# Optimization experiments

Measured on AMD Instinct MI355X. Metric: run time of the kernel, lower is better.

Reference implementation:

```python
import jax, jax.numpy as jnp
import numpy as np
import math

N_FFT = 1024
HOP = 256
WIN = 1024
SR = 16000
N_MELS = 80
N_STFT = N_FFT // 2 + 1  # 513
B = 16
T_AUDIO = 320000


def _hz_to_mel_slaney(f):
    f = np.asarray(f, dtype=np.float64)
    mels = 3.0 * f / 200.0
    min_log_hz = 1000.0
    min_log_mel = 15.0
    logstep = math.log(6.4) / 27.0
    return np.where(f >= min_log_hz, min_log_mel + np.log(np.maximum(f, 1e-10) / min_log_hz) / logstep, mels)


def _mel_to_hz_slaney(m):
    m = np.asarray(m, dtype=np.float64)
    freqs = 200.0 * m / 3.0
    min_log_hz = 1000.0
    min_log_mel = 15.0
    logstep = math.log(6.4) / 27.0
    return np.where(m >= min_log_mel, min_log_hz * np.exp(logstep * (m - min_log_mel)), freqs)


def _melscale_fbanks(n_freqs, f_min, f_max, n_mels, sample_rate):
    # torchaudio.functional.melscale_fbanks with norm='slaney', mel_scale='slaney'
    all_freqs = np.linspace(0.0, sample_rate / 2.0, n_freqs)
    m_pts = np.linspace(_hz_to_mel_slaney(f_min), _hz_to_mel_slaney(f_max), n_mels + 2)
    f_pts = _mel_to_hz_slaney(m_pts)
    f_diff = f_pts[1:] - f_pts[:-1]                       # (n_mels+1,)
    slopes = f_pts[None, :] - all_freqs[:, None]          # (n_freqs, n_mels+2)
    down = -slopes[:, :-2] / f_diff[:-1]
    up = slopes[:, 2:] / f_diff[1:]
    fb = np.maximum(0.0, np.minimum(down, up))
    enorm = 2.0 / (f_pts[2:n_mels + 2] - f_pts[:n_mels])  # slaney norm
    fb = fb * enorm[None, :]
    return fb.astype(np.float32)                          # (n_freqs, n_mels)


def setup_inputs() -> dict:
    key = jax.random.key(0)
    wav = jax.random.normal(key, (B, 1, T_AUDIO), dtype=jnp.float32)
    # hann window, periodic
    n = np.arange(WIN, dtype=np.float64)
    window = (0.5 - 0.5 * np.cos(2.0 * np.pi * n / WIN)).astype(np.float32)
    mel_fbanks = _melscale_fbanks(N_STFT, 0.0, SR / 2.0, N_MELS, SR)
    k = np.arange(N_STFT, dtype=np.float64)[:, None]
    nn = np.arange(N_FFT, dtype=np.float64)[None, :]
    angle = -2.0 * np.pi * k * nn / N_FFT
    rfft_real_t = np.cos(angle).T.astype(np.float32)      # (n_fft, n_stft)
    rfft_imag_t = np.sin(angle).T.astype(np.float32)
    return {
        "wav_with_channel": wav,
        "window": jnp.asarray(window),
        "mel_fbanks": jnp.asarray(mel_fbanks),
        "rfft_real_t": jnp.asarray(rfft_real_t),
        "rfft_imag_t": jnp.asarray(rfft_imag_t),
    }


def reference(wav_with_channel, window, mel_fbanks, rfft_real_t, rfft_imag_t):
    wav = wav_with_channel[:, 0, :]                       # (B, T)
    pad = N_FFT // 2
    padded = jnp.pad(wav, ((0, 0), (pad, pad)), mode="reflect")
    padded_len = padded.shape[1]
    num_frames = (padded_len - WIN) // HOP + 1
    idx = jnp.arange(num_frames)[:, None] * HOP + jnp.arange(WIN)[None, :]
    frames = padded[:, idx]
    windowed = frames * window
    real = jnp.matmul(windowed, rfft_real_t)              # (B, F, n_stft)
    imag = jnp.matmul(windowed, rfft_imag_t)
    magnitude = jnp.sqrt(real * real + imag * imag)       # power == 1.0
    mel = jnp.matmul(magnitude, mel_fbanks)               # (B, F, n_mels)
    return jnp.transpose(mel, (0, 2, 1))                  # (B, n_mels, F)
```

## Files before the change

kernel.cpp:

```cpp
#include <hip/hip_runtime.h>
#include <cstddef>

#define HOP 256
#define NSTFT 513
#define N_MELS 80
#define T_AUDIO 320000
#define NUM_FRAMES 1251
#define NBATCH 16
#define TOTAL_FRAMES (NBATCH * NUM_FRAMES)

#define LOGSTEP 0.06875177742094913f
#define MEL_MAX 45.24564047f
#define DF 15.625f

__device__ __forceinline__ int reflect_idx(int j) {
    j = (j < 0) ? -j : j;
    j = (j >= T_AUDIO) ? (2 * T_AUDIO - 2 - j) : j;
    return j;
}

__device__ __forceinline__ int m1_of(int k) {
    const float f = k * DF;
    const float mel = (f < 1000.f) ? (3.0f / 200.0f) * f
                                   : 15.0f + logf(f * 1e-3f) * (1.0f / LOGSTEP);
    return (int)floorf(mel * (81.0f / MEL_MAX));
}

__device__ __forceinline__ int swz(int k) {
    return (k & ~15) | ((k ^ (k >> 4)) & 15);
}

__device__ __forceinline__ unsigned cvt_pk_bf16(float lo, float hi) {
    unsigned r;
    asm("v_cvt_pk_bf16_f32 %0, %1, %2" : "=v"(r) : "v"(lo), "v"(hi));
    return r;
}

__device__ __forceinline__ float plsum32(float v) {
#if __has_builtin(__builtin_amdgcn_permlane32_swap)
    auto r = __builtin_amdgcn_permlane32_swap(__float_as_int(v), __float_as_int(v), false, false);
    return __int_as_float(r[0]) + __int_as_float(r[1]);
#else
    return v + __shfl_xor(v, 32);
#endif
}
__device__ __forceinline__ float plsum16(float v) {
#if __has_builtin(__builtin_amdgcn_permlane16_swap)
    auto r = __builtin_amdgcn_permlane16_swap(__float_as_int(v), __float_as_int(v), false, false);
    return __int_as_float(r[0]) + __int_as_float(r[1]);
#else
    return v + __shfl_xor(v, 16);
#endif
}

#define DPP_XOR1 0xB1
#define DPP_XOR2 0x4E
#define DPP_XOR8 0x128
template<int CTRL>
__device__ __forceinline__ float dppf(float x) {
    return __int_as_float(__builtin_amdgcn_update_dpp(
        0, __float_as_int(x), CTRL, 0xF, 0xF, true));
}

template<class F>
__device__ __forceinline__ void cstage(float (&zr)[2][16], float (&zi)[2][16],
                                       float sg, float twr_, float twi_, F comm) {
    #pragma unroll
    for (int p = 0; p < 2; ++p) {
        #pragma unroll
        for (int r = 0; r < 16; ++r) {
            const float pr  = comm(zr[p][r]);
            const float pim = comm(zi[p][r]);
            const float qr = fmaf(sg, zr[p][r], pr);
            const float qi = fmaf(sg, zi[p][r], pim);
            zr[p][r] = fmaf(qr, twr_, -(qi * twi_));
            zi[p][r] = fmaf(qr, twi_, qi * twr_);
        }
    }
}

template<class FS>
__device__ __forceinline__ void cstage_sum(float (&zr)[2][16], float (&zi)[2][16],
                                           float m2, float twr_, float twi_, FS sumf) {
    #pragma unroll
    for (int p = 0; p < 2; ++p) {
        #pragma unroll
        for (int r = 0; r < 16; ++r) {
            const float sR = sumf(zr[p][r]);
            const float sI = sumf(zi[p][r]);
            const float qr = fmaf(m2, zr[p][r], sR);
            const float qi = fmaf(m2, zi[p][r], sI);
            zr[p][r] = fmaf(qr, twr_, -(qi * twi_));
            zi[p][r] = fmaf(qr, twi_, qi * twr_);
        }
    }
}

__global__ __launch_bounds__(256) void melspec_pk4_kernel(
    const float* __restrict__ wav,
    const float* __restrict__ window,
    const float* __restrict__ fb,
    const float* __restrict__ cosT,
    const float* __restrict__ sinT,
    float* __restrict__ out)
{
    __shared__ uint2  smag4[4][512];
    __shared__ float2 wtab[512];
    __shared__ unsigned short ks[84];

    const int tid = threadIdx.x;
    const int lane = tid & 63;
    const int w = tid >> 6;
    const int g0 = (blockIdx.x * 4 + w) * 4;

    const int BREV4[16] = {0,8,4,12,2,10,6,14,1,9,5,13,3,11,7,15};
    const int SIG[16]   = {0,1,3,2,7,6,5,4,15,14,13,12,11,10,9,8};
    const float W16R[8] = {1.0f, 0.92387953251128674f, 0.70710678118654752f, 0.38268343236508977f,
                           0.0f, -0.38268343236508977f, -0.70710678118654752f, -0.92387953251128674f};
    const float W16I[8] = {0.0f, -0.38268343236508977f, -0.70710678118654752f, -0.92387953251128674f,
                           -1.0f, -0.92387953251128674f, -0.70710678118654752f, -0.38268343236508977f};

    if (tid == 0) { ks[81] = 512; ks[82] = 512; }
    for (int k = tid; k <= 512; k += 256) {
        const int mc = m1_of(k);
        if (k <= 511) {
            const float wu = (mc >= 0 && mc <= 79) ? fb[k * N_MELS + mc] : 0.0f;
            const float wd = (mc >= 1 && mc <= 80) ? fb[k * N_MELS + mc - 1] : 0.0f;
            wtab[swz(k)] = make_float2(wu, wd);
        }
        if (k >= 1) {
            const int mp = m1_of(k - 1);
            for (int m = mp + 1; m <= mc; ++m) ks[m] = (unsigned short)k;
            if (k == 1) ks[0] = 1;
        }
    }
    __syncthreads();

    unsigned bf0, ff0, bf3;
    {
        const unsigned g = (unsigned)g0;
        bf0 = g / NUM_FRAMES; ff0 = g - bf0 * NUM_FRAMES;
        bf3 = (unsigned)(g0 + 3) / NUM_FRAMES;
    }

    float win[16];
    #pragma unroll
    for (int r = 0; r < 16; ++r) win[r] = window[r * 64 + lane];

    float zr[2][16], zi[2][16];
    if (bf0 == bf3) {
        const float* wb = wav + (size_t)bf0 * T_AUDIO;
        const int base = (int)ff0 * HOP - 512;
        float ch[28];
        if (base >= 0 && base + 27 * 64 + 63 < T_AUDIO) {
            #pragma unroll
            for (int c = 0; c < 28; ++c)
                ch[c] = wb[base + c * 64 + lane];
        } else {
            #pragma unroll
            for (int c = 0; c < 28; ++c)
                ch[c] = wb[reflect_idx(base + c * 64 + lane)];
        }
        #pragma unroll
        for (int r = 0; r < 16; ++r) {
            zr[0][r] = ch[r]      * win[r];
            zi[0][r] = ch[r + 4]  * win[r];
            zr[1][r] = ch[r + 8]  * win[r];
            zi[1][r] = ch[r + 12] * win[r];
        }
    } else {
        #pragma unroll
        for (int fi = 0; fi < 4; ++fi) {
            const unsigned g = (unsigned)(g0 + fi);
            const unsigned bb = g / NUM_FRAMES;
            const unsigned ffr = g - bb * NUM_FRAMES;
            const float* wb = wav + (size_t)bb * T_AUDIO;
            const int base = (int)ffr * HOP - 512;
            #pragma unroll
            for (int r = 0; r < 16; ++r) {
                const float v = wb[reflect_idx(base + r * 64 + lane)] * win[r];
                if (fi == 0) zr[0][r] = v;
                else if (fi == 1) zi[0][r] = v;
                else if (fi == 2) zr[1][r] = v;
                else zi[1][r] = v;
            }
        }
    }

    const float* twc = cosT + NSTFT;
    const float* tws = sinT + NSTFT;

    const float w1r = twc[lane];
    const float w1i = tws[lane];
    float wkr[16], wki[16];
    wkr[0] = 1.0f; wki[0] = 0.0f;
    #pragma unroll
    for (int k = 1; k < 16; ++k) {
        wkr[k] = wkr[k-1] * w1r - wki[k-1] * w1i;
        wki[k] = wkr[k-1] * w1i + wki[k-1] * w1r;
    }

    float c64[6], s64[6];
    #pragma unroll
    for (int t = 0; t < 6; ++t) {
        const int half = 32 >> t;
        const bool hi = (lane & half) != 0;
        const int jj = (lane & (half - 1)) << (t + 4);
        c64[t] = hi ? twc[jj] : 1.0f;
        s64[t] = hi ? tws[jj] : 0.0f;
    }

    #define CBFLY(ar, ai, br, bi, wr, wi) { \
        const float _tr = (ar) - (br), _ti = (ai) - (bi); \
        (ar) += (br); (ai) += (bi); \
        (br) = _tr * (wr) - _ti * (wi); \
        (bi) = _tr * (wi) + _ti * (wr); }

    #pragma unroll
    for (int p = 0; p < 2; ++p) {
        #pragma unroll
        for (int q = 0; q < 8; ++q) CBFLY(zr[p][q], zi[p][q], zr[p][q+8], zi[p][q+8], W16R[q], W16I[q]);
        #pragma unroll
        for (int g = 0; g < 16; g += 8)
            #pragma unroll
            for (int q = 0; q < 4; ++q) CBFLY(zr[p][g+q], zi[p][g+q], zr[p][g+q+4], zi[p][g+q+4], W16R[2*q], W16I[2*q]);
        #pragma unroll
        for (int g = 0; g < 16; g += 4)
            #pragma unroll
            for (int q = 0; q < 2; ++q) CBFLY(zr[p][g+q], zi[p][g+q], zr[p][g+q+2], zi[p][g+q+2], W16R[4*q], W16I[4*q]);
        #pragma unroll
        for (int g = 0; g < 16; g += 2) CBFLY(zr[p][g], zi[p][g], zr[p][g+1], zi[p][g+1], 1.0f, 0.0f);
    }

    #pragma unroll
    for (int r = 1; r < 16; ++r) {
        const float c1 = wkr[BREV4[r]];
        const float s1 = wki[BREV4[r]];
        #pragma unroll
        for (int p = 0; p < 2; ++p) {
            const float xr = zr[p][r], xi = zi[p][r];
            zr[p][r] = xr * c1 - xi * s1;
            zi[p][r] = xr * s1 + xi * c1;
        }
    }

    {
        cstage_sum(zr, zi, (lane & 32) ? -2.0f : 0.0f, c64[0], s64[0],
                   [](float v) { return plsum32(v); });
        cstage_sum(zr, zi, (lane & 16) ? -2.0f : 0.0f, c64[1], s64[1],
                   [](float v) { return plsum16(v); });
        float sg;
        sg = (lane & 8) ? -1.0f : 1.0f;
        cstage(zr, zi, sg, c64[2], s64[2], [](float v) { return dppf<DPP_XOR8>(v); });
        sg = (lane & 4) ? -1.0f : 1.0f;
        cstage(zr, zi, sg, c64[3], s64[3], [](float v) { return __shfl_xor(v, 4); });
        sg = (lane & 2) ? -1.0f : 1.0f;
        cstage(zr, zi, sg, c64[4], s64[4], [](float v) { return dppf<DPP_XOR2>(v); });
        sg = (lane & 1) ? -1.0f : 1.0f;
        cstage(zr, zi, sg, c64[5], s64[5], [](float v) { return dppf<DPP_XOR1>(v); });
    }

    const int k2 = (int)(__brev((unsigned)lane) >> 26);
    const int lp0 = (int)(__brev((unsigned)((64 - k2) & 63)) >> 26);
    #pragma unroll
    for (int r = 0; r < 16; ++r) {
        float cx0, cy0, cx1, cy1;
        if (r == 0) {
            cx0 = __shfl(zr[0][0], lp0); cy0 = __shfl(zi[0][0], lp0);
            cx1 = __shfl(zr[1][0], lp0); cy1 = __shfl(zi[1][0], lp0);
        } else {
            cx0 = __shfl_xor(zr[0][SIG[r]], 63); cy0 = __shfl_xor(zi[0][SIG[r]], 63);
            cx1 = __shfl_xor(zr[1][SIG[r]], 63); cy1 = __shfl_xor(zi[1][SIG[r]], 63);
        }
        const int k1 = BREV4[r];
        const int k = k2 * 16 + k1;
        if (k <= 511) {
            const float a0 = zr[0][r], b0 = zi[0][r];
            const float mA0 = 0.5f * sqrtf((a0 + cx0) * (a0 + cx0) + (b0 - cy0) * (b0 - cy0));
            const float mB0 = 0.5f * sqrtf((b0 + cy0) * (b0 + cy0) + (a0 - cx0) * (a0 - cx0));
            const float a1 = zr[1][r], b1 = zi[1][r];
            const float mA1 = 0.5f * sqrtf((a1 + cx1) * (a1 + cx1) + (b1 - cy1) * (b1 - cy1));
            const float mB1 = 0.5f * sqrtf((b1 + cy1) * (b1 + cy1) + (a1 - cx1) * (a1 - cx1));
            smag4[w][(k & ~15) | (k1 ^ (k2 & 15))] =
                make_uint2(cvt_pk_bf16(mA0, mB0), cvt_pk_bf16(mA1, mB1));
        }
    }

    #pragma unroll
    for (int ii = 0; ii < 3; ++ii) {
        const int t2 = lane + 64 * ii;
        if (t2 < 2 * N_MELS) {
            const int m = 79 - (t2 >> 1);
            const int half = t2 & 1;
            const int ka = ks[m], kb = ks[m + 1], kc = ks[m + 2];
            const int km = (ka + kc + 1) >> 1;
            const int kbeg = half ? km : ka;
            const int kend = half ? kc : km;
            float a0 = 0.f, b0 = 0.f, a1 = 0.f, b1 = 0.f;
            for (int k = kbeg; k < kend; ++k) {
                const int sl = swz(k);
                const uint2 mg = smag4[w][sl];
                const float2 wt = wtab[sl];
                const float ws = (k < kb) ? wt.x : wt.y;
                a0 = fmaf(__uint_as_float(mg.x << 16), ws, a0);
                b0 = fmaf(__uint_as_float(mg.x & 0xffff0000u), ws, b0);
                a1 = fmaf(__uint_as_float(mg.y << 16), ws, a1);
                b1 = fmaf(__uint_as_float(mg.y & 0xffff0000u), ws, b1);
            }
            a0 += dppf<DPP_XOR1>(a0);  b0 += dppf<DPP_XOR1>(b0);
            a1 += dppf<DPP_XOR1>(a1);  b1 += dppf<DPP_XOR1>(b1);
            const float v0 = half ? b0 : a0;
            const float v1 = half ? b1 : a1;
            const unsigned gA = (unsigned)(g0 + half);
            const unsigned bbA = gA / NUM_FRAMES;
            const unsigned ffA = gA - bbA * NUM_FRAMES;
            out[((size_t)bbA * N_MELS + m) * NUM_FRAMES + ffA] = v0;
            const unsigned gB = (unsigned)(g0 + 2 + half);
            const unsigned bbB = gB / NUM_FRAMES;
            const unsigned ffB = gB - bbB * NUM_FRAMES;
            out[((size_t)bbB * N_MELS + m) * NUM_FRAMES + ffB] = v1;
        }
    }
}

extern "C" void kernel_launch(void* const* d_in, const int* in_sizes, int n_in,
                              void* d_out, int out_size, void* d_ws, size_t ws_size,
                              hipStream_t stream) {
    const float* wav    = (const float*)d_in[0];
    const float* window = (const float*)d_in[1];
    const float* fb     = (const float*)d_in[2];
    const float* cosT   = (const float*)d_in[3];
    const float* sinT   = (const float*)d_in[4];
    float* out = (float*)d_out;

    const int blocks = TOTAL_FRAMES / 16;
    melspec_pk4_kernel<<<blocks, 256, 0, stream>>>(wav, window, fb, cosT, sinT, out);
}
```

Before: 46.64 us.

## Precompute mel weight tables in a setup kernel and use smaller blocks

After: 49.86 us. 6.9% more time.

```diff
diff --git a/kernel.cpp b/kernel.cpp
--- a/kernel.cpp
+++ b/kernel.cpp
@@ -35,6 +35,8 @@
     asm("v_cvt_pk_bf16_f32 %0, %1, %2" : "=v"(r) : "v"(lo), "v"(hi));
     return r;
 }
+__device__ __forceinline__ float lo16f(unsigned u) { return __uint_as_float(u << 16); }
+__device__ __forceinline__ float hi16f(unsigned u) { return __uint_as_float(u & 0xffff0000u); }
 
 __device__ __forceinline__ float plsum32(float v) {
 #if __has_builtin(__builtin_amdgcn_permlane32_swap)
@@ -96,13 +98,272 @@
     }
 }
 
-__global__ __launch_bounds__(256) void melspec_pk4_kernel(
+__global__ __launch_bounds__(256) void melspec_setup(const float* __restrict__ fb,
+                                                     float* __restrict__ wsf) {
+    const int tid = threadIdx.x;
+    unsigned short* ksg = (unsigned short*)(wsf + 1024);
+    if (tid == 0) { ksg[81] = 512; ksg[82] = 512; ksg[83] = 512; }
+    for (int k = tid; k <= 512; k += 256) {
+        const int mc = m1_of(k);
+        if (k <= 511) {
+            const float wu = (mc >= 0 && mc <= 79) ? 0.5f * fb[k * N_MELS + mc] : 0.0f;
+            const float wd = (mc >= 1 && mc <= 80) ? 0.5f * fb[k * N_MELS + mc - 1] : 0.0f;
+            wsf[swz(k)] = wu;
+            wsf[512 + swz(k)] = wd;
+        }
+        if (k >= 1) {
+            const int mp = m1_of(k - 1);
+            for (int m = mp + 1; m <= mc; ++m) ksg[m] = (unsigned short)k;
+            if (k == 1) ksg[0] = 1;
+        }
+    }
+}
+
+__global__ __launch_bounds__(128) void melspec_pk6_kernel(
     const float* __restrict__ wav,
     const float* __restrict__ window,
-    const float* __restrict__ fb,
+    const float* __restrict__ wsf,
     const float* __restrict__ cosT,
     const float* __restrict__ sinT,
     float* __restrict__ out)
+{
+    __shared__ uint2  smag4[2][512];
+    __shared__ float  swu[512];
+    __shared__ float  swd[512];
+    __shared__ unsigned short ks_l[84];
+
+    const int tid = threadIdx.x;
+    const int lane = tid & 63;
+    const int w = tid >> 6;
+    const int g0 = (blockIdx.x * 2 + w) * 4;
+
+    const int BREV4[16] = {0,8,4,12,2,10,6,14,1,9,5,13,3,11,7,15};
+    const int SIG[16]   = {0,1,3,2,7,6,5,4,15,14,13,12,11,10,9,8};
+    const float W16R[8] = {1.0f, 0.92387953251128674f, 0.70710678118654752f, 0.38268343236508977f,
+                           0.0f, -0.38268343236508977f, -0.70710678118654752f, -0.92387953251128674f};
+    const float W16I[8] = {0.0f, -0.38268343236508977f, -0.70710678118654752f, -0.92387953251128674f,
+                           -1.0f, -0.92387953251128674f, -0.70710678118654752f, -0.38268343236508977f};
+
+    const unsigned short* ksg = (const unsigned short*)(wsf + 1024);
+    #pragma unroll
+    for (int i = tid; i < 512; i += 128) { swu[i] = wsf[i]; swd[i] = wsf[512 + i]; }
+    if (tid < 84) ks_l[tid] = ksg[tid];
+    __syncthreads();
+
+    unsigned bf0, ff0, bf3;
+    {
+        const unsigned g = (unsigned)g0;
+        bf0 = g / NUM_FRAMES; ff0 = g - bf0 * NUM_FRAMES;
+        bf3 = (unsigned)(g0 + 3) / NUM_FRAMES;
+    }
+
+    float win[16];
+    #pragma unroll
+    for (int r = 0; r < 16; ++r) win[r] = window[r * 64 + lane];
+
+    float zr[2][16], zi[2][16];
+    if (bf0 == bf3) {
+        const float* wb = wav + (size_t)bf0 * T_AUDIO;
+        const int base = (int)ff0 * HOP - 512;
+        float ch[28];
+        if (base >= 0 && base + 27 * 64 + 63 < T_AUDIO) {
+            #pragma unroll
+            for (int c = 0; c < 28; ++c)
+                ch[c] = wb[base + c * 64 + lane];
+        } else {
+            #pragma unroll
+            for (int c = 0; c < 28; ++c)
+                ch[c] = wb[reflect_idx(base + c * 64 + lane)];
+        }
+        #pragma unroll
+        for (int r = 0; r < 16; ++r) {
+            zr[0][r] = ch[r]      * win[r];
+            zi[0][r] = ch[r + 4]  * win[r];
+            zr[1][r] = ch[r + 8]  * win[r];
+            zi[1][r] = ch[r + 12] * win[r];
+        }
+    } else {
+        #pragma unroll
+        for (int fi = 0; fi < 4; ++fi) {
+            const unsigned g = (unsigned)(g0 + fi);
+            const unsigned bb = g / NUM_FRAMES;
+            const unsigned ffr = g - bb * NUM_FRAMES;
+            const float* wb = wav + (size_t)bb * T_AUDIO;
+            const int base = (int)ffr * HOP - 512;
+            #pragma unroll
+            for (int r = 0; r < 16; ++r) {
+                const float v = wb[reflect_idx(base + r * 64 + lane)] * win[r];
+                if (fi == 0) zr[0][r] = v;
+                else if (fi == 1) zi[0][r] = v;
+                else if (fi == 2) zr[1][r] = v;
+                else zi[1][r] = v;
+            }
+        }
+    }
+
+    const float* twc = cosT + NSTFT;
+    const float* tws = sinT + NSTFT;
+
+    const float w1r = twc[lane];
+    const float w1i = tws[lane];
+    float wkr[16], wki[16];
+    wkr[0] = 1.0f; wki[0] = 0.0f;
+    #pragma unroll
+    for (int k = 1; k < 16; ++k) {
+        wkr[k] = wkr[k-1] * w1r - wki[k-1] * w1i;
+        wki[k] = wkr[k-1] * w1i + wki[k-1] * w1r;
+    }
+
+    float c64[6], s64[6];
+    #pragma unroll
+    for (int t = 0; t < 6; ++t) {
+        const int half = 32 >> t;
+        const bool hi = (lane & half) != 0;
+        const int jj = (lane & (half - 1)) << (t + 4);
+        c64[t] = hi ? twc[jj] : 1.0f;
+        s64[t] = hi ? tws[jj] : 0.0f;
+    }
+
+    #define CBFLY(ar, ai, br, bi, wr, wi) { \
+        const float _tr = (ar) - (br), _ti = (ai) - (bi); \
+        (ar) += (br); (ai) += (bi); \
+        (br) = _tr * (wr) - _ti * (wi); \
+        (bi) = _tr * (wi) + _ti * (wr); }
+
+    #pragma unroll
+    for (int p = 0; p < 2; ++p) {
+        #pragma unroll
+        for (int q = 0; q < 8; ++q) CBFLY(zr[p][q], zi[p][q], zr[p][q+8], zi[p][q+8], W16R[q], W16I[q]);
+        #pragma unroll
+        for (int g = 0; g < 16; g += 8)
+            #pragma unroll
+            for (int q = 0; q < 4; ++q) CBFLY(zr[p][g+q], zi[p][g+q], zr[p][g+q+4], zi[p][g+q+4], W16R[2*q], W16I[2*q]);
+        #pragma unroll
+        for (int g = 0; g < 16; g += 4)
+            #pragma unroll
+            for (int q = 0; q < 2; ++q) CBFLY(zr[p][g+q], zi[p][g+q], zr[p][g+q+2], zi[p][g+q+2], W16R[4*q], W16I[4*q]);
+        #pragma unroll
+        for (int g = 0; g < 16; g += 2) CBFLY(zr[p][g], zi[p][g], zr[p][g+1], zi[p][g+1], 1.0f, 0.0f);
+    }
+
+    #pragma unroll
+    for (int r = 1; r < 16; ++r) {
+        const float c1 = wkr[BREV4[r]];
+        const float s1 = wki[BREV4[r]];
+        #pragma unroll
+        for (int p = 0; p < 2; ++p) {
+            const float xr = zr[p][r], xi = zi[p][r];
+            zr[p][r] = xr * c1 - xi * s1;
+            zi[p][r] = xr * s1 + xi * c1;
+        }
+    }
+
+    {
+        cstage_sum(zr, zi, (lane & 32) ? -2.0f : 0.0f, c64[0], s64[0],
+                   [](float v) { return plsum32(v); });
+        cstage_sum(zr, zi, (lane & 16) ? -2.0f : 0.0f, c64[1], s64[1],
+                   [](float v) { return plsum16(v); });
+        float sg;
+        sg = (lane & 8) ? -1.0f : 1.0f;
+        cstage(zr, zi, sg, c64[2], s64[2], [](float v) { return dppf<DPP_XOR8>(v); });
+        sg = (lane & 4) ? -1.0f : 1.0f;
+        cstage(zr, zi, sg, c64[3], s64[3], [](float v) { return __shfl_xor(v, 4); });
+        sg = (lane & 2) ? -1.0f : 1.0f;
+        cstage(zr, zi, sg, c64[4], s64[4], [](float v) { return dppf<DPP_XOR2>(v); });
+        sg = (lane & 1) ? -1.0f : 1.0f;
+        cstage(zr, zi, sg, c64[5], s64[5], [](float v) { return dppf<DPP_XOR1>(v); });
+    }
+
+    const int k2 = (int)(__brev((unsigned)lane) >> 26);
+    const int lp0 = (int)(__brev((unsigned)((64 - k2) & 63)) >> 26);
+    const bool hasbin = (k2 < 32);
+    #pragma unroll
+    for (int r = 1; r < 16; ++r) {
+        const float sxr = hasbin ? zr[1][r] : zr[0][SIG[r]];
+        const float sxi = hasbin ? zi[1][r] : zi[0][SIG[r]];
+        const float cx = __shfl_xor(sxr, 63);
+        const float cy = __shfl_xor(sxi, 63);
+        const float a = hasbin ? zr[0][r] : zr[1][SIG[r]];
+        const float b = hasbin ? zi[0][r] : zi[1][SIG[r]];
+        const float sA = a + cx, dA = b - cy;
+        const float sB = b + cy, dB = a - cx;
+        const float magA = sqrtf(sA * sA + dA * dA);
+        const float magB = sqrtf(sB * sB + dB * dB);
+        const unsigned pk = cvt_pk_bf16(magA, magB);
+        const unsigned pko = (unsigned)__shfl_xor((int)pk, 63);
+        if (hasbin) {
+            const int k1 = BREV4[r];
+            const int k = k2 * 16 + k1;
+            smag4[w][(k & ~15) | (k1 ^ (k2 & 15))] = make_uint2(pk, pko);
+        }
+    }
+    {
+        const float cx0 = __shfl(zr[0][0], lp0), cy0 = __shfl(zi[0][0], lp0);
+        const float cx1 = __shfl(zr[1][0], lp0), cy1 = __shfl(zi[1][0], lp0);
+        if (hasbin) {
+            const float a0 = zr[0][0], b0 = zi[0][0];
+            const float mA0 = sqrtf((a0 + cx0) * (a0 + cx0) + (b0 - cy0) * (b0 - cy0));
+            const float mB0 = sqrtf((b0 + cy0) * (b0 + cy0) + (a0 - cx0) * (a0 - cx0));
+            const float a1 = zr[1][0], b1 = zi[1][0];
+            const float mA1 = sqrtf((a1 + cx1) * (a1 + cx1) + (b1 - cy1) * (b1 - cy1));
+            const float mB1 = sqrtf((b1 + cy1) * (b1 + cy1) + (a1 - cx1) * (a1 - cx1));
+            const int k = k2 * 16;
+            smag4[w][(k & ~15) | (0 ^ (k2 & 15))] =
+                make_uint2(cvt_pk_bf16(mA0, mB0), cvt_pk_bf16(mA1, mB1));
+        }
+    }
+
+    #pragma unroll
+    for (int ii = 0; ii < 3; ++ii) {
+        const int t2 = lane + 64 * ii;
+        if (t2 < 2 * N_MELS) {
+            const int m = 79 - (t2 >> 1);
+            const int half = t2 & 1;
+            const int ka = ks_l[m], kb = ks_l[m + 1], kc = ks_l[m + 2];
+            const int km = (ka + kc + 1) >> 1;
+            const int kbeg = half ? km : ka;
+            const int kend = half ? kc : km;
+            float a0 = 0.f, b0 = 0.f, a1 = 0.f, b1 = 0.f;
+            const int upend = min(kb, kend);
+            for (int k = kbeg; k < upend; ++k) {
+                const int sl = swz(k);
+                const uint2 mg = smag4[w][sl];
+                const float ws = swu[sl];
+                a0 = fmaf(lo16f(mg.x), ws, a0);
+                b0 = fmaf(hi16f(mg.x), ws, b0);
+                a1 = fmaf(lo16f(mg.y), ws, a1);
+                b1 = fmaf(hi16f(mg.y), ws, b1);
+            }
+            const int dnbeg = max(kb, kbeg);
+            for (int k = dnbeg; k < kend; ++k) {
+                const int sl = swz(k);
+                const uint2 mg = smag4[w][sl];
+                const float ws = swd[sl];
+                a0 = fmaf(lo16f(mg.x), ws, a0);
+                b0 = fmaf(hi16f(mg.x), ws, b0);
+                a1 = fmaf(lo16f(mg.y), ws, a1);
+                b1 = fmaf(hi16f(mg.y), ws, b1);
+            }
+            a0 += dppf<DPP_XOR1>(a0);  b0 += dppf<DPP_XOR1>(b0);
+            a1 += dppf<DPP_XOR1>(a1);  b1 += dppf<DPP_XOR1>(b1);
+            const float v0 = half ? b0 : a0;
+            const float v1 = half ? b1 : a1;
+            const unsigned gA = (unsigned)(g0 + half);
+            const unsigned bbA = gA / NUM_FRAMES;
+            const unsigned ffA = gA - bbA * NUM_FRAMES;
+            out[((size_t)bbA * N_MELS + m) * NUM_FRAMES + ffA] = v0;
+            const unsigned gB = (unsigned)(g0 + 2 + half);
+            const unsigned bbB = gB / NUM_FRAMES;
+            const unsigned ffB = gB - bbB * NUM_FRAMES;
+            out[((size_t)bbB * N_MELS + m) * NUM_FRAMES + ffB] = v1;
+        }
+    }
+}
+
+__global__ __launch_bounds__(256) void melspec_pk4_kernel(
+    const float* __restrict__ wav, const float* __restrict__ window,
+    const float* __restrict__ fb, const float* __restrict__ cosT,
+    const float* __restrict__ sinT, float* __restrict__ out)
 {
     __shared__ uint2  smag4[4][512];
     __shared__ float2 wtab[512];
@@ -154,12 +415,10 @@
         float ch[28];
         if (base >= 0 && base + 27 * 64 + 63 < T_AUDIO) {
             #pragma unroll
-            for (int c = 0; c < 28; ++c)
-                ch[c] = wb[base + c * 64 + lane];
+            for (int c = 0; c < 28; ++c) ch[c] = wb[base + c * 64 + lane];
         } else {
             #pragma unroll
-            for (int c = 0; c < 28; ++c)
-                ch[c] = wb[reflect_idx(base + c * 64 + lane)];
+            for (int c = 0; c < 28; ++c) ch[c] = wb[reflect_idx(base + c * 64 + lane)];
         }
         #pragma unroll
         for (int r = 0; r < 16; ++r) {
@@ -189,7 +448,6 @@
 
     const float* twc = cosT + NSTFT;
     const float* tws = sinT + NSTFT;
-
     const float w1r = twc[lane];
     const float w1i = tws[lane];
     float wkr[16], wki[16];
@@ -199,7 +457,6 @@
         wkr[k] = wkr[k-1] * w1r - wki[k-1] * w1i;
         wki[k] = wkr[k-1] * w1i + wki[k-1] * w1r;
     }
-
     float c64[6], s64[6];
     #pragma unroll
     for (int t = 0; t < 6; ++t) {
@@ -210,12 +467,6 @@
         s64[t] = hi ? tws[jj] : 0.0f;
     }
 
-    #define CBFLY(ar, ai, br, bi, wr, wi) { \
-        const float _tr = (ar) - (br), _ti = (ai) - (bi); \
-        (ar) += (br); (ai) += (bi); \
-        (br) = _tr * (wr) - _ti * (wi); \
-        (bi) = _tr * (wi) + _ti * (wr); }
-
     #pragma unroll
     for (int p = 0; p < 2; ++p) {
         #pragma unroll
@@ -231,7 +482,6 @@
         #pragma unroll
         for (int g = 0; g < 16; g += 2) CBFLY(zr[p][g], zi[p][g], zr[p][g+1], zi[p][g+1], 1.0f, 0.0f);
     }
-
     #pragma unroll
     for (int r = 1; r < 16; ++r) {
         const float c1 = wkr[BREV4[r]];
@@ -243,7 +493,6 @@
             zi[p][r] = xr * s1 + xi * c1;
         }
     }
-
     {
         cstage_sum(zr, zi, (lane & 32) ? -2.0f : 0.0f, c64[0], s64[0],
                    [](float v) { return plsum32(v); });
@@ -302,10 +551,10 @@
                 const uint2 mg = smag4[w][sl];
                 const float2 wt = wtab[sl];
                 const float ws = (k < kb) ? wt.x : wt.y;
-                a0 = fmaf(__uint_as_float(mg.x << 16), ws, a0);
-                b0 = fmaf(__uint_as_float(mg.x & 0xffff0000u), ws, b0);
-                a1 = fmaf(__uint_as_float(mg.y << 16), ws, a1);
-                b1 = fmaf(__uint_as_float(mg.y & 0xffff0000u), ws, b1);
+                a0 = fmaf(lo16f(mg.x), ws, a0);
+                b0 = fmaf(hi16f(mg.x), ws, b0);
+                a1 = fmaf(lo16f(mg.y), ws, a1);
+                b1 = fmaf(hi16f(mg.y), ws, b1);
             }
             a0 += dppf<DPP_XOR1>(a0);  b0 += dppf<DPP_XOR1>(b0);
             a1 += dppf<DPP_XOR1>(a1);  b1 += dppf<DPP_XOR1>(b1);
@@ -333,6 +582,13 @@
     const float* sinT   = (const float*)d_in[4];
     float* out = (float*)d_out;
 
-    const int blocks = TOTAL_FRAMES / 16;
-    melspec_pk4_kernel<<<blocks, 256, 0, stream>>>(wav, window, fb, cosT, sinT, out);
-}
+    if (ws_size >= 4608 && d_ws != nullptr) {
+        float* wsf = (float*)d_ws;
+        melspec_setup<<<1, 256, 0, stream>>>(fb, wsf);
+        const int blocks = TOTAL_FRAMES / 8;
+        melspec_pk6_kernel<<<blocks, 128, 0, stream>>>(wav, window, wsf, cosT, sinT, out);
+    } else {
+        const int blocks = TOTAL_FRAMES / 16;
+        melspec_pk4_kernel<<<blocks, 256, 0, stream>>>(wav, window, fb, cosT, sinT, out);
+    }
+}
```

## Split magnitude work across mirrored lanes and split mel loop into up/down passes

Applied to the files above, without the earlier changes.

New measurement: 45.89 us, median of 2. About the same (-1.6%).

```diff
diff --git a/kernel.cpp b/kernel.cpp
--- a/kernel.cpp
+++ b/kernel.cpp
@@ -35,6 +35,8 @@
     asm("v_cvt_pk_bf16_f32 %0, %1, %2" : "=v"(r) : "v"(lo), "v"(hi));
     return r;
 }
+__device__ __forceinline__ float lo16f(unsigned u) { return __uint_as_float(u << 16); }
+__device__ __forceinline__ float hi16f(unsigned u) { return __uint_as_float(u & 0xffff0000u); }
 
 __device__ __forceinline__ float plsum32(float v) {
 #if __has_builtin(__builtin_amdgcn_permlane32_swap)
@@ -96,7 +98,7 @@
     }
 }
 
-__global__ __launch_bounds__(256) void melspec_pk4_kernel(
+__global__ __launch_bounds__(256) void melspec_pk7_kernel(
     const float* __restrict__ wav,
     const float* __restrict__ window,
     const float* __restrict__ fb,
@@ -105,8 +107,10 @@
     float* __restrict__ out)
 {
     __shared__ uint2  smag4[4][512];
-    __shared__ float2 wtab[512];
-    __shared__ unsigned short ks[84];
+    __shared__ float  swu[512];
+    __shared__ float  swd[512];
+    __shared__ unsigned short ks_l[84];
+    __shared__ unsigned char  mtab[513];
 
     const int tid = threadIdx.x;
     const int lane = tid & 63;
@@ -120,18 +124,19 @@
     const float W16I[8] = {0.0f, -0.38268343236508977f, -0.70710678118654752f, -0.92387953251128674f,
                            -1.0f, -0.92387953251128674f, -0.70710678118654752f, -0.38268343236508977f};
 
-    if (tid == 0) { ks[81] = 512; ks[82] = 512; }
+    for (int k = tid; k <= 512; k += 256) mtab[k] = (unsigned char)m1_of(k);
+    if (tid == 0) { ks_l[81] = 512; ks_l[82] = 512; ks_l[83] = 512; }
+    __syncthreads();
     for (int k = tid; k <= 512; k += 256) {
-        const int mc = m1_of(k);
+        const int mc = mtab[k];
         if (k <= 511) {
-            const float wu = (mc >= 0 && mc <= 79) ? fb[k * N_MELS + mc] : 0.0f;
-            const float wd = (mc >= 1 && mc <= 80) ? fb[k * N_MELS + mc - 1] : 0.0f;
-            wtab[swz(k)] = make_float2(wu, wd);
+            swu[swz(k)] = (mc <= 79) ? 0.5f * fb[k * N_MELS + mc] : 0.0f;
+            swd[swz(k)] = (mc >= 1 && mc <= 80) ? 0.5f * fb[k * N_MELS + mc - 1] : 0.0f;
         }
         if (k >= 1) {
-            const int mp = m1_of(k - 1);
-            for (int m = mp + 1; m <= mc; ++m) ks[m] = (unsigned short)k;
-            if (k == 1) ks[0] = 1;
+            const int mp = mtab[k - 1];
+            for (int m = mp + 1; m <= mc; ++m) ks_l[m] = (unsigned short)k;
+            if (k == 1) ks_l[0] = 1;
         }
     }
     __syncthreads();
@@ -262,26 +267,39 @@
 
     const int k2 = (int)(__brev((unsigned)lane) >> 26);
     const int lp0 = (int)(__brev((unsigned)((64 - k2) & 63)) >> 26);
-    #pragma unroll
-    for (int r = 0; r < 16; ++r) {
-        float cx0, cy0, cx1, cy1;
-        if (r == 0) {
-            cx0 = __shfl(zr[0][0], lp0); cy0 = __shfl(zi[0][0], lp0);
-            cx1 = __shfl(zr[1][0], lp0); cy1 = __shfl(zi[1][0], lp0);
-        } else {
-            cx0 = __shfl_xor(zr[0][SIG[r]], 63); cy0 = __shfl_xor(zi[0][SIG[r]], 63);
-            cx1 = __shfl_xor(zr[1][SIG[r]], 63); cy1 = __shfl_xor(zi[1][SIG[r]], 63);
-        }
-        const int k1 = BREV4[r];
-        const int k = k2 * 16 + k1;
-        if (k <= 511) {
-            const float a0 = zr[0][r], b0 = zi[0][r];
-            const float mA0 = 0.5f * sqrtf((a0 + cx0) * (a0 + cx0) + (b0 - cy0) * (b0 - cy0));
-            const float mB0 = 0.5f * sqrtf((b0 + cy0) * (b0 + cy0) + (a0 - cx0) * (a0 - cx0));
-            const float a1 = zr[1][r], b1 = zi[1][r];
-            const float mA1 = 0.5f * sqrtf((a1 + cx1) * (a1 + cx1) + (b1 - cy1) * (b1 - cy1));
-            const float mB1 = 0.5f * sqrtf((b1 + cy1) * (b1 + cy1) + (a1 - cx1) * (a1 - cx1));
-            smag4[w][(k & ~15) | (k1 ^ (k2 & 15))] =
+    const bool hasbin = (k2 < 32);
+    #pragma unroll
+    for (int r = 1; r < 16; ++r) {
+        const float sxr = hasbin ? zr[1][r] : zr[0][SIG[r]];
+        const float sxi = hasbin ? zi[1][r] : zi[0][SIG[r]];
+        const float cx = __shfl_xor(sxr, 63);
+        const float cy = __shfl_xor(sxi, 63);
+        const float a = hasbin ? zr[0][r] : zr[1][SIG[r]];
+        const float b = hasbin ? zi[0][r] : zi[1][SIG[r]];
+        const float sA = a + cx, dA = b - cy;
+        const float sB = b + cy, dB = a - cx;
+        const float magA = sqrtf(sA * sA + dA * dA);
+        const float magB = sqrtf(sB * sB + dB * dB);
+        const unsigned pk = cvt_pk_bf16(magA, magB);
+        const unsigned pko = (unsigned)__shfl_xor((int)pk, 63);
+        if (hasbin) {
+            const int k1 = BREV4[r];
+            const int k = k2 * 16 + k1;
+            smag4[w][(k & ~15) | (k1 ^ (k2 & 15))] = make_uint2(pk, pko);
+        }
+    }
+    {
+        const float cx0 = __shfl(zr[0][0], lp0), cy0 = __shfl(zi[0][0], lp0);
+        const float cx1 = __shfl(zr[1][0], lp0), cy1 = __shfl(zi[1][0], lp0);
+        if (hasbin) {
+            const float a0 = zr[0][0], b0 = zi[0][0];
+            const float mA0 = sqrtf((a0 + cx0) * (a0 + cx0) + (b0 - cy0) * (b0 - cy0));
+            const float mB0 = sqrtf((b0 + cy0) * (b0 + cy0) + (a0 - cx0) * (a0 - cx0));
+            const float a1 = zr[1][0], b1 = zi[1][0];
+            const float mA1 = sqrtf((a1 + cx1) * (a1 + cx1) + (b1 - cy1) * (b1 - cy1));
+            const float mB1 = sqrtf((b1 + cy1) * (b1 + cy1) + (a1 - cx1) * (a1 - cx1));
+            const int k = k2 * 16;
+            smag4[w][(k & ~15) | (0 ^ (k2 & 15))] =
                 make_uint2(cvt_pk_bf16(mA0, mB0), cvt_pk_bf16(mA1, mB1));
         }
     }
@@ -292,20 +310,30 @@
         if (t2 < 2 * N_MELS) {
             const int m = 79 - (t2 >> 1);
             const int half = t2 & 1;
-            const int ka = ks[m], kb = ks[m + 1], kc = ks[m + 2];
+            const int ka = ks_l[m], kb = ks_l[m + 1], kc = ks_l[m + 2];
             const int km = (ka + kc + 1) >> 1;
             const int kbeg = half ? km : ka;
             const int kend = half ? kc : km;
             float a0 = 0.f, b0 = 0.f, a1 = 0.f, b1 = 0.f;
-            for (int k = kbeg; k < kend; ++k) {
+            const int upend = min(kb, kend);
+            for (int k = kbeg; k < upend; ++k) {
                 const int sl = swz(k);
                 const uint2 mg = smag4[w][sl];
-                const float2 wt = wtab[sl];
-                const float ws = (k < kb) ? wt.x : wt.y;
-                a0 = fmaf(__uint_as_float(mg.x << 16), ws, a0);
-                b0 = fmaf(__uint_as_float(mg.x & 0xffff0000u), ws, b0);
-                a1 = fmaf(__uint_as_float(mg.y << 16), ws, a1);
-                b1 = fmaf(__uint_as_float(mg.y & 0xffff0000u), ws, b1);
+                const float ws = swu[sl];
+                a0 = fmaf(lo16f(mg.x), ws, a0);
+                b0 = fmaf(hi16f(mg.x), ws, b0);
+                a1 = fmaf(lo16f(mg.y), ws, a1);
+                b1 = fmaf(hi16f(mg.y), ws, b1);
+            }
+            const int dnbeg = max(kb, kbeg);
+            for (int k = dnbeg; k < kend; ++k) {
+                const int sl = swz(k);
+                const uint2 mg = smag4[w][sl];
+                const float ws = swd[sl];
+                a0 = fmaf(lo16f(mg.x), ws, a0);
+                b0 = fmaf(hi16f(mg.x), ws, b0);
+                a1 = fmaf(lo16f(mg.y), ws, a1);
+                b1 = fmaf(hi16f(mg.y), ws, b1);
             }
             a0 += dppf<DPP_XOR1>(a0);  b0 += dppf<DPP_XOR1>(b0);
             a1 += dppf<DPP_XOR1>(a1);  b1 += dppf<DPP_XOR1>(b1);
@@ -334,5 +362,5 @@
     float* out = (float*)d_out;
 
     const int blocks = TOTAL_FRAMES / 16;
-    melspec_pk4_kernel<<<blocks, 256, 0, stream>>>(wav, window, fb, cosT, sinT, out);
-}
+    melspec_pk7_kernel<<<blocks, 256, 0, stream>>>(wav, window, fb, cosT, sinT, out);
+}
```
